# Performance work log

Measured on AMD Instinct MI355X. Metric: run time of the kernel, lower is better.

Reference implementation:

```python
import jax, jax.numpy as jnp
import numpy as np
from jax import lax

D = 96        # voxel grid side
C = 16        # code_dim == inner channels
NCONV = 17    # total conv layers in the net
DN = ('NCDHW', 'OIDHW', 'NCDHW')
PAD1 = [(1, 1)] * 3


def _bn_relu_mask(y, s, b, mask):
    # eval-mode BN folded to scale/bias, ReLU, then restrict to active voxels
    s = s[None, :, None, None, None]
    b = b[None, :, None, None, None]
    return jnp.maximum(y * s + b, 0.0) * mask


def _subm(x, mask, w, s, b):
    # SubMConv3d: dense 3x3x3 conv on zero-padded sparse features, output only at
    # the (unchanged) active sites -> conv + mask is exactly equal math.
    y = lax.conv_general_dilated(x, w, (1, 1, 1), PAD1, dimension_numbers=DN)
    return _bn_relu_mask(y, s, b, mask)


def _down(x, mask, w, s, b):
    # SparseConv3d stride 2, pad 1: output active wherever any input in the 3^3
    # window is active (= max-pool of the mask).
    y = lax.conv_general_dilated(x, w, (2, 2, 2), PAD1, dimension_numbers=DN)
    new_mask = lax.reduce_window(mask, 0.0, lax.max, (1, 1, 3, 3, 3),
                                 (1, 1, 2, 2, 2),
                                 [(0, 0), (0, 0), (1, 1), (1, 1), (1, 1)])
    return _bn_relu_mask(y, s, b, new_mask), new_mask


def setup_inputs() -> dict:
    key = jax.random.key(0)
    k1, k2, k3, k4, k5 = jax.random.split(key, 5)
    mask_idx = jax.random.randint(k1, (1, 1, D, D, D), 0, 10, dtype=jnp.int32)
    mask = (mask_idx == 0).astype(jnp.float32)
    x = jax.random.normal(k2, (1, C, D, D, D), jnp.float32) * mask
    # 0.05 ~ 1/sqrt(27*16): keeps activations sane over 17 layers
    W = jax.random.normal(k3, (NCONV, C, C, 3, 3, 3), jnp.float32) * 0.05
    bn_scale = jax.random.uniform(k4, (NCONV, C), jnp.float32, 0.5, 1.5)
    bn_bias = jax.random.normal(k5, (NCONV, C), jnp.float32) * 0.1
    return {"x": x, "mask_idx": mask_idx, "W": W,
            "bn_scale": bn_scale, "bn_bias": bn_bias}


def reference(x, mask_idx, W, bn_scale, bn_bias):
    mask = (mask_idx == 0).astype(x.dtype)
    net = x
    i = 0
    # conv0: double_conv at full res
    for _ in range(2):
        net = _subm(net, mask, W[i], bn_scale[i], bn_bias[i]); i += 1
    # down0
    net, mask = _down(net, mask, W[i], bn_scale[i], bn_bias[i]); i += 1
    # conv1: double_conv -> net1.dense()
    for _ in range(2):
        net = _subm(net, mask, W[i], bn_scale[i], bn_bias[i]); i += 1
    net1 = net
    # down1 + conv2 (triple) -> net2
    net, mask = _down(net, mask, W[i], bn_scale[i], bn_bias[i]); i += 1
    for _ in range(3):
        net = _subm(net, mask, W[i], bn_scale[i], bn_bias[i]); i += 1
    net2 = net
    # down2 + conv3 (triple) -> net3
    net, mask = _down(net, mask, W[i], bn_scale[i], bn_bias[i]); i += 1
    for _ in range(3):
        net = _subm(net, mask, W[i], bn_scale[i], bn_bias[i]); i += 1
    net3 = net
    # down3 + conv4 (triple) -> net4
    net, mask = _down(net, mask, W[i], bn_scale[i], bn_bias[i]); i += 1
    for _ in range(3):
        net = _subm(net, mask, W[i], bn_scale[i], bn_bias[i]); i += 1
    net4 = net
    return (net1, net2, net3, net4)
```

## Files before the change

### kernel.cpp

```cpp
#include <hip/hip_runtime.h>

#define C 16
#define TAPS 27
#define NCONV 17
#define LISTCAP 98304
#define NPAIR 14

typedef _Float16 half8 __attribute__((ext_vector_type(8)));
typedef _Float16 half4 __attribute__((ext_vector_type(4)));
typedef float f32x4 __attribute__((ext_vector_type(4)));

__global__ void prep_kernel(const float* __restrict__ x, const int* __restrict__ mask_idx,
                            _Float16* __restrict__ P0h, _Float16* __restrict__ P1h,
                            const float* __restrict__ W, _Float16* __restrict__ Wh,
                            int* __restrict__ counts, float* __restrict__ m48) {
    const int n96 = 96 * 96 * 96;
    int b = blockIdx.x;
    if (b < 3456) {
        int v = b * 256 + threadIdx.x;
        half8 h0, h1;
#pragma unroll
        for (int c = 0; c < 8; c++) h0[c] = (_Float16)x[(long)c * n96 + v];
#pragma unroll
        for (int c = 0; c < 8; c++) h1[c] = (_Float16)x[(long)(c + 8) * n96 + v];
        half8* dp = reinterpret_cast<half8*>(P0h + (long)v * C);
        dp[0] = h0;
        dp[1] = h1;
        half8 zz = {};
        half8* zp = reinterpret_cast<half8*>(P1h + (long)v * C);
        zp[0] = zz;
        zp[1] = zz;
        int act = (mask_idx[v] == 0);
        unsigned long long bl = __ballot(act);
        __shared__ int wsum[4];
        int wid = threadIdx.x >> 6, lane = threadIdx.x & 63;
        if (lane == 0) wsum[wid] = __popcll(bl);
        __syncthreads();
        if (threadIdx.x == 0) counts[b] = wsum[0] + wsum[1] + wsum[2] + wsum[3];
    } else if (b < 3456 + 476) {
        int i = (b - 3456) * 256 + threadIdx.x;
        const int total = NCONV * NPAIR * 64 * 8;
        if (i < total) {
            int j = i & 7;
            int lane = (i >> 3) & 63;
            int p = (i >> 9) % NPAIR;
            int l = (i >> 9) / NPAIR;
            int co = lane & 15;
            int g = lane >> 4;
            int k = 8 * g + j;
            int ci = k & 15;
            int tap = 2 * p + (k >> 4);
            float val = (tap < TAPS) ? W[((l * C + co) * C + ci) * TAPS + tap] : 0.f;
            Wh[i] = (_Float16)val;
        }
    } else {
        int i = (b - 3456 - 476) * 256 + threadIdx.x;
        int xx = i % 48, yy = (i / 48) % 48, zc = i / (48 * 48);
        float m = 0.f;
        for (int dz = 0; dz < 3; dz++) {
            int z2 = 2 * zc - 1 + dz;
            if ((unsigned)z2 >= 96u) continue;
            for (int dy = 0; dy < 3; dy++) {
                int y2 = 2 * yy - 1 + dy;
                if ((unsigned)y2 >= 96u) continue;
                for (int dx = 0; dx < 3; dx++) {
                    int x2 = 2 * xx - 1 + dx;
                    if ((unsigned)x2 >= 96u) continue;
                    if (mask_idx[((long)z2 * 96 + y2) * 96 + x2] == 0) m = 1.f;
                }
            }
        }
        m48[i] = m;
    }
}

__global__ void scan_kernel(const int* __restrict__ counts, int* __restrict__ offsets,
                            int* __restrict__ nact, int nb) {
    __shared__ int s[256];
    int t = threadIdx.x;
    const int CH = (nb + 255) / 256;
    int base = t * CH, sum = 0;
    for (int j = 0; j < CH; j++)
        if (base + j < nb) sum += counts[base + j];
    s[t] = sum;
    __syncthreads();
    for (int off = 1; off < 256; off <<= 1) {
        int v = (t >= off) ? s[t - off] : 0;
        __syncthreads();
        s[t] += v;
        __syncthreads();
    }
    int run = s[t] - sum;
    for (int j = 0; j < CH; j++) {
        if (base + j < nb) {
            offsets[base + j] = run;
            run += counts[base + j];
        }
    }
    if (t == 255) *nact = s[255];
}

__global__ void scatter_kernel(const int* __restrict__ mi, const int* __restrict__ offsets,
                               int* __restrict__ list, int cap, const float* __restrict__ m48,
                               float* __restrict__ m24, float* __restrict__ m12,
                               float* __restrict__ m6) {
    int b = blockIdx.x;
    int tid = threadIdx.x;
    if (b < 3456) {
        int i = b * 256 + tid;
        int act = (mi[i] == 0);
        unsigned long long bl = __ballot(act);
        __shared__ int wsum[4];
        int wid = tid >> 6, lane = tid & 63;
        if (lane == 0) wsum[wid] = __popcll(bl);
        __syncthreads();
        int wbase = 0;
        for (int w = 0; w < wid; w++) wbase += wsum[w];
        int prefix = __popcll(bl & ((1ull << lane) - 1));
        if (act) {
            int pos = offsets[b] + wbase + prefix;
            if (pos < cap) list[pos] = i;
        }
    } else if (b < 3456 + 54) {
        int i = (b - 3456) * 256 + tid;
        if (i < 24 * 24 * 24) {
            int x = i % 24, y = (i / 24) % 24, z = i / (24 * 24);
            float m = 0.f;
            for (int dz = 0; dz < 3; dz++) {
                int zz = 2 * z - 1 + dz;
                if ((unsigned)zz >= 48u) continue;
                for (int dy = 0; dy < 3; dy++) {
                    int yy = 2 * y - 1 + dy;
                    if ((unsigned)yy >= 48u) continue;
                    for (int dx = 0; dx < 3; dx++) {
                        int xx = 2 * x - 1 + dx;
                        if ((unsigned)xx >= 48u) continue;
                        m = fmaxf(m, m48[((long)zz * 48 + yy) * 48 + xx]);
                    }
                }
            }
            m24[i] = m;
        }
    } else if (b < 3456 + 54 + 432) {
        int wv = (b - 3456 - 54) * 4 + (tid >> 6);
        int lane = tid & 63;
        int x = wv % 12, y = (wv / 12) % 12, z = wv / 144;
        float m = 0.f;
        for (int k = lane; k < 343; k += 64) {
            int dz = k / 49, r = k % 49, dy = r / 7, dx = r % 7;
            int zz = 4 * z - 3 + dz, yy = 4 * y - 3 + dy, xx = 4 * x - 3 + dx;
            if ((unsigned)zz < 48u && (unsigned)yy < 48u && (unsigned)xx < 48u)
                m = fmaxf(m, m48[((long)zz * 48 + yy) * 48 + xx]);
        }
        for (int off = 32; off; off >>= 1) m = fmaxf(m, __shfl_xor(m, off));
        if (lane == 0 && wv < 1728) m12[wv] = m;
    } else {
        int wv = (b - 3456 - 54 - 432) * 4 + (tid >> 6);
        int lane = tid & 63;
        int x = wv % 6, y = (wv / 6) % 6, z = wv / 36;
        float m = 0.f;
        for (int k = lane; k < 3375; k += 64) {
            int dz = k / 225, r = k % 225, dy = r / 15, dx = r % 15;
            int zz = 8 * z - 7 + dz, yy = 8 * y - 7 + dy, xx = 8 * x - 7 + dx;
            if ((unsigned)zz < 48u && (unsigned)yy < 48u && (unsigned)xx < 48u)
                m = fmaxf(m, m48[((long)zz * 48 + yy) * 48 + xx]);
        }
        for (int off = 32; off; off >>= 1) m = fmaxf(m, __shfl_xor(m, off));
        if (lane == 0 && wv < 216) m6[wv] = m;
    }
}

template <int STRIDE, bool SPARSE, bool WF32>
__global__ __launch_bounds__(256) void mconv_kernel(
    const _Float16* __restrict__ in, _Float16* __restrict__ out,
    const float* __restrict__ mask, const int* __restrict__ list,
    const int* __restrict__ nact, const _Float16* __restrict__ Whl,
    const float* __restrict__ bs, const float* __restrict__ bb,
    int Din, int Dout, float* __restrict__ outf) {
    int n = Dout * Dout * Dout;
    int nv;
    if (SPARSE) {
        nv = *nact;
        if (nv > LISTCAP) nv = LISTCAP;
    } else {
        nv = n;
    }
    int tile = blockIdx.x * 4 + (threadIdx.x >> 6);
    if (tile * 16 >= nv) return;

    int lane = threadIdx.x & 63;
    int col = lane & 15;
    int g = lane >> 4;
    int s = tile * 16 + col;
    bool val = s < nv;
    int v = 0;
    if (SPARSE) {
        if (val) v = list[s];
    } else {
        v = val ? s : 0;
    }
    int x = v % Dout, y = (v / Dout) % Dout, z = v / (Dout * Dout);

    const half8* wf = reinterpret_cast<const half8*>(Whl);
    half8 a[NPAIR];
#pragma unroll
    for (int p = 0; p < NPAIR; p++) a[p] = wf[p * 64 + lane];

    int half_off = (g & 1) * 8;
    int tg = g >> 1;

    f32x4 acc = {0.f, 0.f, 0.f, 0.f};
#pragma unroll
    for (int p = 0; p < NPAIR; p++) {
        int tap = 2 * p + tg;
        if (tap > TAPS - 1) tap = TAPS - 1;
        int kz = tap / 9, ky = (tap / 3) % 3, kx = tap % 3;
        int zz = STRIDE * z - 1 + kz;
        int yy = STRIDE * y - 1 + ky;
        int xx = STRIDE * x - 1 + kx;
        bool ok = val && ((unsigned)zz < (unsigned)Din) && ((unsigned)yy < (unsigned)Din) &&
                  ((unsigned)xx < (unsigned)Din);
        half8 b = {};
        if (ok) {
            b = *reinterpret_cast<const half8*>(
                in + (long)((zz * Din + yy) * Din + xx) * C + half_off);
        }
        acc = __builtin_amdgcn_mfma_f32_16x16x32_f16(a[p], b, acc, 0, 0, 0);
    }

    if (val) {
        float mk = SPARSE ? 1.f : mask[v];
        int cob = g * 4;
        half4 r;
#pragma unroll
        for (int j = 0; j < 4; j++) {
            float t = fmaxf(acc[j] * bs[cob + j] + bb[cob + j], 0.f) * mk;
            r[j] = (_Float16)t;
            if (WF32) outf[(long)(cob + j) * n + v] = t;
        }
        *reinterpret_cast<half4*>(out + (long)v * C + cob) = r;
    }
}

__global__ __launch_bounds__(1024) void tail6_kernel(
    const _Float16* __restrict__ gin,
    const float* __restrict__ m6, const _Float16* __restrict__ Wh,
    const float* __restrict__ bs, const float* __restrict__ bb,
    float* __restrict__ out4) {
    __shared__ _Float16 G0[216 * 16], G1[216 * 16];
    __shared__ float Lm6[216];

    int tid = threadIdx.x;
    int lane = tid & 63;
    int wid = tid >> 6;
    int col = lane & 15, g = lane >> 4;
    int ho = (g & 1) * 8, tg = g >> 1;

    for (int i = tid; i < 216; i += 1024) Lm6[i] = m6[i];
    __syncthreads();

    int s = wid * 16 + col;
    bool val = (wid < 14) && (s < 216);
    int v = val ? s : 0;
    int x = v % 6, y = (v / 6) % 6, z = v / 36;

    auto layer = [&](const _Float16* gsrc, const _Float16* lsrc, int Din, int stride,
                     int lidx, _Float16* lout, float* outf) {
        const half8* wf = reinterpret_cast<const half8*>(Wh + (long)lidx * NPAIR * 64 * 8);
        half8 a[NPAIR];
#pragma unroll
        for (int p = 0; p < NPAIR; p++) a[p] = wf[p * 64 + lane];
        f32x4 acc = {0.f, 0.f, 0.f, 0.f};
#pragma unroll
        for (int p = 0; p < NPAIR; p++) {
            int tap = 2 * p + tg;
            if (tap > TAPS - 1) tap = TAPS - 1;
            int kz = tap / 9, ky = (tap / 3) % 3, kx = tap % 3;
            int zz = stride * z - 1 + kz;
            int yy = stride * y - 1 + ky;
            int xx = stride * x - 1 + kx;
            bool ok = val && ((unsigned)zz < (unsigned)Din) && ((unsigned)yy < (unsigned)Din) &&
                      ((unsigned)xx < (unsigned)Din);
            half8 b = {};
            if (ok) {
                long off = (long)((zz * Din + yy) * Din + xx) * C + ho;
                b = gsrc ? *reinterpret_cast<const half8*>(gsrc + off)
                         : *reinterpret_cast<const half8*>(lsrc + off);
            }
            acc = __builtin_amdgcn_mfma_f32_16x16x32_f16(a[p], b, acc, 0, 0, 0);
        }
        if (val) {
            float mkv = Lm6[v];
            int cob = g * 4;
            const float* bsl = bs + lidx * C;
            const float* bbl = bb + lidx * C;
            half4 r;
#pragma unroll
            for (int j = 0; j < 4; j++) {
                float t = fmaxf(acc[j] * bsl[cob + j] + bbl[cob + j], 0.f) * mkv;
                r[j] = (_Float16)t;
                if (outf) outf[(long)(cob + j) * 216 + v] = t;
            }
            if (lout) *reinterpret_cast<half4*>(lout + (long)v * C + cob) = r;
        }
        __syncthreads();
    };

    layer(gin, nullptr, 12, 2, 13, G0, nullptr);
    layer(nullptr, G0, 6, 1, 14, G1, nullptr);
    layer(nullptr, G1, 6, 1, 15, G0, nullptr);
    layer(nullptr, G0, 6, 1, 16, nullptr, out4);
}

extern "C" void kernel_launch(void* const* d_in, const int* in_sizes, int n_in,
                              void* d_out, int out_size, void* d_ws, size_t ws_size,
                              hipStream_t stream) {
    const float* x = (const float*)d_in[0];
    const int* mask_idx = (const int*)d_in[1];
    const float* W = (const float*)d_in[2];
    const float* bs = (const float*)d_in[3];
    const float* bb = (const float*)d_in[4];
    float* out = (float*)d_out;

    const int n96 = 96 * 96 * 96;
    const int n48 = 48 * 48 * 48;
    const int n24 = 24 * 24 * 24;
    const int n12 = 12 * 12 * 12;
    const int n6 = 6 * 6 * 6;
    const int NB = 3456;

    _Float16* P0h = (_Float16*)d_ws;
    _Float16* P1h = P0h + (long)C * n96;
    float* m48 = (float*)(P1h + (long)C * n96);
    float* m24 = m48 + n48;
    float* m12 = m24 + n24;
    float* m6 = m12 + n12;
    _Float16* Wh = (_Float16*)(m6 + n6);
    int* list = (int*)(Wh + (long)NCONV * NPAIR * 64 * 8);
    int* counts = list + LISTCAP;
    int* offsets = counts + NB;
    int* nact = offsets + NB;

    hipLaunchKernelGGL(prep_kernel, dim3(3456 + 476 + 432), dim3(256), 0, stream,
                       x, mask_idx, P0h, P1h, W, Wh, counts, m48);
    hipLaunchKernelGGL(scan_kernel, dim3(1), dim3(256), 0, stream, counts, offsets, nact, NB);
    hipLaunchKernelGGL(scatter_kernel, dim3(3456 + 54 + 432 + 54), dim3(256), 0, stream,
                       mask_idx, offsets, list, LISTCAP, m48, m24, m12, m6);

    auto mblk = [&](long nvox) { return dim3((unsigned)((nvox + 63) / 64)); };
    auto WL = [&](int l) { return Wh + (long)l * NPAIR * 64 * 8; };

    hipLaunchKernelGGL((mconv_kernel<1, true, false>), mblk(LISTCAP), dim3(256), 0, stream,
                       P0h, P1h, (const float*)nullptr, list, nact, WL(0), bs, bb, 96, 96,
                       (float*)nullptr);
    hipLaunchKernelGGL((mconv_kernel<1, true, false>), mblk(LISTCAP), dim3(256), 0, stream,
                       P1h, P0h, (const float*)nullptr, list, nact, WL(1), bs + C, bb + C, 96, 96,
                       (float*)nullptr);
    hipLaunchKernelGGL((mconv_kernel<2, false, false>), mblk(n48), dim3(256), 0, stream,
                       P0h, P1h, m48, list, nact, WL(2), bs + 2 * C, bb + 2 * C, 96, 48,
                       (float*)nullptr);
    hipLaunchKernelGGL((mconv_kernel<1, false, false>), mblk(n48), dim3(256), 0, stream,
                       P1h, P0h, m48, list, nact, WL(3), bs + 3 * C, bb + 3 * C, 48, 48,
                       (float*)nullptr);
    hipLaunchKernelGGL((mconv_kernel<1, false, true>), mblk(n48), dim3(256), 0, stream,
                       P0h, P1h, m48, list, nact, WL(4), bs + 4 * C, bb + 4 * C, 48, 48,
                       out);
    hipLaunchKernelGGL((mconv_kernel<2, false, false>), mblk(n24), dim3(256), 0, stream,
                       P1h, P0h, m24, list, nact, WL(5), bs + 5 * C, bb + 5 * C, 48, 24,
                       (float*)nullptr);
    hipLaunchKernelGGL((mconv_kernel<1, false, false>), mblk(n24), dim3(256), 0, stream,
                       P0h, P1h, m24, list, nact, WL(6), bs + 6 * C, bb + 6 * C, 24, 24,
                       (float*)nullptr);
    hipLaunchKernelGGL((mconv_kernel<1, false, false>), mblk(n24), dim3(256), 0, stream,
                       P1h, P0h, m24, list, nact, WL(7), bs + 7 * C, bb + 7 * C, 24, 24,
                       (float*)nullptr);
    hipLaunchKernelGGL((mconv_kernel<1, false, true>), mblk(n24), dim3(256), 0, stream,
                       P0h, P1h, m24, list, nact, WL(8), bs + 8 * C, bb + 8 * C, 24, 24,
                       out + (long)C * n48);
    hipLaunchKernelGGL((mconv_kernel<2, false, false>), mblk(n12), dim3(256), 0, stream,
                       P1h, P0h, m12, list, nact, WL(9), bs + 9 * C, bb + 9 * C, 24, 12,
                       (float*)nullptr);
    hipLaunchKernelGGL((mconv_kernel<1, false, false>), mblk(n12), dim3(256), 0, stream,
                       P0h, P1h, m12, list, nact, WL(10), bs + 10 * C, bb + 10 * C, 12, 12,
                       (float*)nullptr);
    hipLaunchKernelGGL((mconv_kernel<1, false, false>), mblk(n12), dim3(256), 0, stream,
                       P1h, P0h, m12, list, nact, WL(11), bs + 11 * C, bb + 11 * C, 12, 12,
                       (float*)nullptr);
    hipLaunchKernelGGL((mconv_kernel<1, false, true>), mblk(n12), dim3(256), 0, stream,
                       P0h, P1h, m12, list, nact, WL(12), bs + 12 * C, bb + 12 * C, 12, 12,
                       out + (long)C * (n48 + n24));
    hipLaunchKernelGGL(tail6_kernel, dim3(1), dim3(1024), 0, stream,
                       P1h, m6, Wh, bs, bb, out + (long)C * (n48 + n24 + n12));
}
```

Baseline: 204.2 us.

## Use compact active-voxel storage with precomputed neighbor table for full-res convs

Replaces the dense 96^3 fp16 feature buffers with compact per-active-voxel arrays. An inverse index map and a 27-tap neighbor table are built once and shared by both full-resolution submanifold convs. The first downsample conv gathers through the inverse map. This removes the dense conversion and zero-fill of two 96^3x16 buffers and the scattered dense gathers, at the cost of an extra compaction kernel, a large neighbor table, and initialising a 96^3 int inverse map.

```diff
diff --git a/kernel.cpp b/kernel.cpp
--- a/kernel.cpp
+++ b/kernel.cpp
@@ -10,35 +10,12 @@
 typedef _Float16 half4 __attribute__((ext_vector_type(4)));
 typedef float f32x4 __attribute__((ext_vector_type(4)));
 
-__global__ void prep_kernel(const float* __restrict__ x, const int* __restrict__ mask_idx,
-                            _Float16* __restrict__ P0h, _Float16* __restrict__ P1h,
-                            const float* __restrict__ W, _Float16* __restrict__ Wh,
-                            int* __restrict__ counts, float* __restrict__ m48) {
-    const int n96 = 96 * 96 * 96;
+__global__ void prep_kernel(const int* __restrict__ mask_idx, const float* __restrict__ W,
+                            _Float16* __restrict__ Wh, int* __restrict__ counts,
+                            float* __restrict__ m48, int* __restrict__ inv) {
     int b = blockIdx.x;
-    if (b < 3456) {
-        int v = b * 256 + threadIdx.x;
-        half8 h0, h1;
-#pragma unroll
-        for (int c = 0; c < 8; c++) h0[c] = (_Float16)x[(long)c * n96 + v];
-#pragma unroll
-        for (int c = 0; c < 8; c++) h1[c] = (_Float16)x[(long)(c + 8) * n96 + v];
-        half8* dp = reinterpret_cast<half8*>(P0h + (long)v * C);
-        dp[0] = h0;
-        dp[1] = h1;
-        half8 zz = {};
-        half8* zp = reinterpret_cast<half8*>(P1h + (long)v * C);
-        zp[0] = zz;
-        zp[1] = zz;
-        int act = (mask_idx[v] == 0);
-        unsigned long long bl = __ballot(act);
-        __shared__ int wsum[4];
-        int wid = threadIdx.x >> 6, lane = threadIdx.x & 63;
-        if (lane == 0) wsum[wid] = __popcll(bl);
-        __syncthreads();
-        if (threadIdx.x == 0) counts[b] = wsum[0] + wsum[1] + wsum[2] + wsum[3];
-    } else if (b < 3456 + 476) {
-        int i = (b - 3456) * 256 + threadIdx.x;
+    if (b < 476) {
+        int i = b * 256 + threadIdx.x;
         const int total = NCONV * NPAIR * 64 * 8;
         if (i < total) {
             int j = i & 7;
@@ -53,8 +30,8 @@
             float val = (tap < TAPS) ? W[((l * C + co) * C + ci) * TAPS + tap] : 0.f;
             Wh[i] = (_Float16)val;
         }
-    } else {
-        int i = (b - 3456 - 476) * 256 + threadIdx.x;
+    } else if (b < 476 + 432) {
+        int i = (b - 476) * 256 + threadIdx.x;
         int xx = i % 48, yy = (i / 48) % 48, zc = i / (48 * 48);
         float m = 0.f;
         for (int dz = 0; dz < 3; dz++) {
@@ -71,6 +48,16 @@
             }
         }
         m48[i] = m;
+    } else {
+        int v = (b - 476 - 432) * 256 + threadIdx.x;
+        inv[v] = -1;
+        int act = (mask_idx[v] == 0);
+        unsigned long long bl = __ballot(act);
+        __shared__ int wsum[4];
+        int wid = threadIdx.x >> 6, lane = threadIdx.x & 63;
+        if (lane == 0) wsum[wid] = __popcll(bl);
+        __syncthreads();
+        if (threadIdx.x == 0) counts[b - 476 - 432] = wsum[0] + wsum[1] + wsum[2] + wsum[3];
     }
 }
 
@@ -101,9 +88,9 @@
 }
 
 __global__ void scatter_kernel(const int* __restrict__ mi, const int* __restrict__ offsets,
-                               int* __restrict__ list, int cap, const float* __restrict__ m48,
-                               float* __restrict__ m24, float* __restrict__ m12,
-                               float* __restrict__ m6) {
+                               int* __restrict__ list, int* __restrict__ inv, int cap,
+                               const float* __restrict__ m48, float* __restrict__ m24,
+                               float* __restrict__ m12, float* __restrict__ m6) {
     int b = blockIdx.x;
     int tid = threadIdx.x;
     if (b < 3456) {
@@ -119,7 +106,10 @@
         int prefix = __popcll(bl & ((1ull << lane) - 1));
         if (act) {
             int pos = offsets[b] + wbase + prefix;
-            if (pos < cap) list[pos] = i;
+            if (pos < cap) {
+                list[pos] = i;
+                inv[i] = pos;
+            }
         }
     } else if (b < 3456 + 54) {
         int i = (b - 3456) * 256 + tid;
@@ -170,21 +160,41 @@
     }
 }
 
-template <int STRIDE, bool SPARSE, bool WF32>
-__global__ __launch_bounds__(256) void mconv_kernel(
-    const _Float16* __restrict__ in, _Float16* __restrict__ out,
-    const float* __restrict__ mask, const int* __restrict__ list,
-    const int* __restrict__ nact, const _Float16* __restrict__ Whl,
-    const float* __restrict__ bs, const float* __restrict__ bb,
-    int Din, int Dout, float* __restrict__ outf) {
-    int n = Dout * Dout * Dout;
-    int nv;
-    if (SPARSE) {
-        nv = *nact;
-        if (nv > LISTCAP) nv = LISTCAP;
-    } else {
-        nv = n;
-    }
+__global__ void compactx_kernel(const float* __restrict__ x, const int* __restrict__ list,
+                                const int* __restrict__ nact, const int* __restrict__ inv,
+                                _Float16* __restrict__ Xc, int* __restrict__ nbr) {
+    const int n96 = 96 * 96 * 96;
+    int nv = *nact;
+    if (nv > LISTCAP) nv = LISTCAP;
+    int s = blockIdx.x * 256 + threadIdx.x;
+    if (s >= nv) return;
+    int v = list[s];
+    half8 h0, h1;
+#pragma unroll
+    for (int c = 0; c < 8; c++) h0[c] = (_Float16)x[(long)c * n96 + v];
+#pragma unroll
+    for (int c = 0; c < 8; c++) h1[c] = (_Float16)x[(long)(c + 8) * n96 + v];
+    half8* dp = reinterpret_cast<half8*>(Xc + (long)s * C);
+    dp[0] = h0;
+    dp[1] = h1;
+    int xx = v % 96, yy = (v / 96) % 96, zz = v / (96 * 96);
+    for (int t = 0; t < TAPS; t++) {
+        int kz = t / 9, ky = (t / 3) % 3, kx = t % 3;
+        int z2 = zz - 1 + kz, y2 = yy - 1 + ky, x2 = xx - 1 + kx;
+        int idx = -1;
+        if ((unsigned)z2 < 96u && (unsigned)y2 < 96u && (unsigned)x2 < 96u)
+            idx = inv[((long)z2 * 96 + y2) * 96 + x2];
+        nbr[t * LISTCAP + s] = idx;
+    }
+}
+
+__global__ __launch_bounds__(256) void sconv_kernel(
+    const _Float16* __restrict__ Ain, _Float16* __restrict__ Aout,
+    const int* __restrict__ nbr, const int* __restrict__ nact,
+    const _Float16* __restrict__ Whl, const float* __restrict__ bs,
+    const float* __restrict__ bb) {
+    int nv = *nact;
+    if (nv > LISTCAP) nv = LISTCAP;
     int tile = blockIdx.x * 4 + (threadIdx.x >> 6);
     if (tile * 16 >= nv) return;
 
@@ -193,12 +203,98 @@
     int g = lane >> 4;
     int s = tile * 16 + col;
     bool val = s < nv;
-    int v = 0;
-    if (SPARSE) {
-        if (val) v = list[s];
-    } else {
-        v = val ? s : 0;
-    }
+
+    const half8* wf = reinterpret_cast<const half8*>(Whl);
+    half8 a[NPAIR];
+#pragma unroll
+    for (int p = 0; p < NPAIR; p++) a[p] = wf[p * 64 + lane];
+
+    int half_off = (g & 1) * 8;
+    int tg = g >> 1;
+
+    f32x4 acc = {0.f, 0.f, 0.f, 0.f};
+#pragma unroll
+    for (int p = 0; p < NPAIR; p++) {
+        int tap = 2 * p + tg;
+        if (tap > TAPS - 1) tap = TAPS - 1;
+        int idx = -1;
+        if (val) idx = nbr[tap * LISTCAP + s];
+        half8 b = {};
+        if (idx >= 0) b = *reinterpret_cast<const half8*>(Ain + (long)idx * C + half_off);
+        acc = __builtin_amdgcn_mfma_f32_16x16x32_f16(a[p], b, acc, 0, 0, 0);
+    }
+
+    if (val) {
+        int cob = g * 4;
+        half4 r;
+#pragma unroll
+        for (int j = 0; j < 4; j++)
+            r[j] = (_Float16)fmaxf(acc[j] * bs[cob + j] + bb[cob + j], 0.f);
+        *reinterpret_cast<half4*>(Aout + (long)s * C + cob) = r;
+    }
+}
+
+__global__ __launch_bounds__(256) void dconv_inv_kernel(
+    const _Float16* __restrict__ Ain, _Float16* __restrict__ out,
+    const float* __restrict__ mask, const int* __restrict__ inv,
+    const _Float16* __restrict__ Whl, const float* __restrict__ bs,
+    const float* __restrict__ bb) {
+    const int n = 48 * 48 * 48;
+    int tile = blockIdx.x * 4 + (threadIdx.x >> 6);
+    if (tile * 16 >= n) return;
+    int lane = threadIdx.x & 63;
+    int col = lane & 15;
+    int g = lane >> 4;
+    int v = tile * 16 + col;
+    int x = v % 48, y = (v / 48) % 48, z = v / (48 * 48);
+
+    const half8* wf = reinterpret_cast<const half8*>(Whl);
+    half8 a[NPAIR];
+#pragma unroll
+    for (int p = 0; p < NPAIR; p++) a[p] = wf[p * 64 + lane];
+    int half_off = (g & 1) * 8;
+    int tg = g >> 1;
+
+    f32x4 acc = {0.f, 0.f, 0.f, 0.f};
+#pragma unroll
+    for (int p = 0; p < NPAIR; p++) {
+        int tap = 2 * p + tg;
+        if (tap > TAPS - 1) tap = TAPS - 1;
+        int kz = tap / 9, ky = (tap / 3) % 3, kx = tap % 3;
+        int zz = 2 * z - 1 + kz, yy = 2 * y - 1 + ky, xx = 2 * x - 1 + kx;
+        int idx = -1;
+        if ((unsigned)zz < 96u && (unsigned)yy < 96u && (unsigned)xx < 96u)
+            idx = inv[((long)zz * 96 + yy) * 96 + xx];
+        half8 b = {};
+        if (idx >= 0) b = *reinterpret_cast<const half8*>(Ain + (long)idx * C + half_off);
+        acc = __builtin_amdgcn_mfma_f32_16x16x32_f16(a[p], b, acc, 0, 0, 0);
+    }
+
+    float mk = mask[v];
+    int cob = g * 4;
+    half4 r;
+#pragma unroll
+    for (int j = 0; j < 4; j++)
+        r[j] = (_Float16)(fmaxf(acc[j] * bs[cob + j] + bb[cob + j], 0.f) * mk);
+    *reinterpret_cast<half4*>(out + (long)v * C + cob) = r;
+}
+
+template <int STRIDE, bool WF32>
+__global__ __launch_bounds__(256) void mconv_kernel(
+    const _Float16* __restrict__ in, _Float16* __restrict__ out,
+    const float* __restrict__ mask, const _Float16* __restrict__ Whl,
+    const float* __restrict__ bs, const float* __restrict__ bb,
+    int Din, int Dout, float* __restrict__ outf) {
+    int n = Dout * Dout * Dout;
+    int tile = blockIdx.x * 4 + (threadIdx.x >> 6);
+    if (tile * 16 >= n) return;
+
+    int lane = threadIdx.x & 63;
+    int col = lane & 15;
+    int g = lane >> 4;
+    int s = tile * 16 + col;
+    bool val = s < n;
+    int v = val ? s : 0;
     int x = v % Dout, y = (v / Dout) % Dout, z = v / (Dout * Dout);
 
     const half8* wf = reinterpret_cast<const half8*>(Whl);
@@ -229,7 +325,7 @@
     }
 
     if (val) {
-        float mk = SPARSE ? 1.f : mask[v];
+        float mk = mask[v];
         int cob = g * 4;
         half4 r;
 #pragma unroll
@@ -243,10 +339,9 @@
 }
 
 __global__ __launch_bounds__(1024) void tail6_kernel(
-    const _Float16* __restrict__ gin,
-    const float* __restrict__ m6, const _Float16* __restrict__ Wh,
-    const float* __restrict__ bs, const float* __restrict__ bb,
-    float* __restrict__ out4) {
+    const _Float16* __restrict__ gin, const float* __restrict__ m6,
+    const _Float16* __restrict__ Wh, const float* __restrict__ bs,
+    const float* __restrict__ bb, float* __restrict__ out4) {
     __shared__ _Float16 G0[216 * 16], G1[216 * 16];
     __shared__ float Lm6[216];
 
@@ -329,9 +424,7 @@
     const int n6 = 6 * 6 * 6;
     const int NB = 3456;
 
-    _Float16* P0h = (_Float16*)d_ws;
-    _Float16* P1h = P0h + (long)C * n96;
-    float* m48 = (float*)(P1h + (long)C * n96);
+    float* m48 = (float*)d_ws;
     float* m24 = m48 + n48;
     float* m12 = m24 + n24;
     float* m6 = m12 + n12;
@@ -340,54 +433,51 @@
     int* counts = list + LISTCAP;
     int* offsets = counts + NB;
     int* nact = offsets + NB;
-
-    hipLaunchKernelGGL(prep_kernel, dim3(3456 + 476 + 432), dim3(256), 0, stream,
-                       x, mask_idx, P0h, P1h, W, Wh, counts, m48);
+    int* inv = nact + 1;
+    int* nbr = inv + n96;
+    _Float16* Xc = (_Float16*)(nbr + TAPS * LISTCAP);
+    _Float16* A1 = Xc + (long)LISTCAP * C;
+    _Float16* A2 = A1 + (long)LISTCAP * C;
+    _Float16* P0h = A2 + (long)LISTCAP * C;
+    _Float16* P1h = P0h + (long)n48 * C;
+
+    hipLaunchKernelGGL(prep_kernel, dim3(476 + 432 + 3456), dim3(256), 0, stream,
+                       mask_idx, W, Wh, counts, m48, inv);
     hipLaunchKernelGGL(scan_kernel, dim3(1), dim3(256), 0, stream, counts, offsets, nact, NB);
     hipLaunchKernelGGL(scatter_kernel, dim3(3456 + 54 + 432 + 54), dim3(256), 0, stream,
-                       mask_idx, offsets, list, LISTCAP, m48, m24, m12, m6);
+                       mask_idx, offsets, list, inv, LISTCAP, m48, m24, m12, m6);
+    hipLaunchKernelGGL(compactx_kernel, dim3(LISTCAP / 256), dim3(256), 0, stream,
+                       x, list, nact, inv, Xc, nbr);
 
     auto mblk = [&](long nvox) { return dim3((unsigned)((nvox + 63) / 64)); };
     auto WL = [&](int l) { return Wh + (long)l * NPAIR * 64 * 8; };
 
-    hipLaunchKernelGGL((mconv_kernel<1, true, false>), mblk(LISTCAP), dim3(256), 0, stream,
-                       P0h, P1h, (const float*)nullptr, list, nact, WL(0), bs, bb, 96, 96,
-                       (float*)nullptr);
-    hipLaunchKernelGGL((mconv_kernel<1, true, false>), mblk(LISTCAP), dim3(256), 0, stream,
-                       P1h, P0h, (const float*)nullptr, list, nact, WL(1), bs + C, bb + C, 96, 96,
-                       (float*)nullptr);
-    hipLaunchKernelGGL((mconv_kernel<2, false, false>), mblk(n48), dim3(256), 0, stream,
-                       P0h, P1h, m48, list, nact, WL(2), bs + 2 * C, bb + 2 * C, 96, 48,
-                       (float*)nullptr);
-    hipLaunchKernelGGL((mconv_kernel<1, false, false>), mblk(n48), dim3(256), 0, stream,
-                       P1h, P0h, m48, list, nact, WL(3), bs + 3 * C, bb + 3 * C, 48, 48,
-                       (float*)nullptr);
-    hipLaunchKernelGGL((mconv_kernel<1, false, true>), mblk(n48), dim3(256), 0, stream,
-                       P0h, P1h, m48, list, nact, WL(4), bs + 4 * C, bb + 4 * C, 48, 48,
-                       out);
-    hipLaunchKernelGGL((mconv_kernel<2, false, false>), mblk(n24), dim3(256), 0, stream,
-                       P1h, P0h, m24, list, nact, WL(5), bs + 5 * C, bb + 5 * C, 48, 24,
-                       (float*)nullptr);
-    hipLaunchKernelGGL((mconv_kernel<1, false, false>), mblk(n24), dim3(256), 0, stream,
-                       P0h, P1h, m24, list, nact, WL(6), bs + 6 * C, bb + 6 * C, 24, 24,
-                       (float*)nullptr);
-    hipLaunchKernelGGL((mconv_kernel<1, false, false>), mblk(n24), dim3(256), 0, stream,
-                       P1h, P0h, m24, list, nact, WL(7), bs + 7 * C, bb + 7 * C, 24, 24,
-                       (float*)nullptr);
-    hipLaunchKernelGGL((mconv_kernel<1, false, true>), mblk(n24), dim3(256), 0, stream,
-                       P0h, P1h, m24, list, nact, WL(8), bs + 8 * C, bb + 8 * C, 24, 24,
-                       out + (long)C * n48);
-    hipLaunchKernelGGL((mconv_kernel<2, false, false>), mblk(n12), dim3(256), 0, stream,
-                       P1h, P0h, m12, list, nact, WL(9), bs + 9 * C, bb + 9 * C, 24, 12,
-                       (float*)nullptr);
-    hipLaunchKernelGGL((mconv_kernel<1, false, false>), mblk(n12), dim3(256), 0, stream,
-                       P0h, P1h, m12, list, nact, WL(10), bs + 10 * C, bb + 10 * C, 12, 12,
-                       (float*)nullptr);
-    hipLaunchKernelGGL((mconv_kernel<1, false, false>), mblk(n12), dim3(256), 0, stream,
-                       P1h, P0h, m12, list, nact, WL(11), bs + 11 * C, bb + 11 * C, 12, 12,
-                       (float*)nullptr);
-    hipLaunchKernelGGL((mconv_kernel<1, false, true>), mblk(n12), dim3(256), 0, stream,
-                       P0h, P1h, m12, list, nact, WL(12), bs + 12 * C, bb + 12 * C, 12, 12,
+    hipLaunchKernelGGL(sconv_kernel, mblk(LISTCAP), dim3(256), 0, stream,
+                       Xc, A1, nbr, nact, WL(0), bs, bb);
+    hipLaunchKernelGGL(sconv_kernel, mblk(LISTCAP), dim3(256), 0, stream,
+                       A1, A2, nbr, nact, WL(1), bs + C, bb + C);
+    hipLaunchKernelGGL(dconv_inv_kernel, mblk(n48), dim3(256), 0, stream,
+                       A2, P1h, m48, inv, WL(2), bs + 2 * C, bb + 2 * C);
+    hipLaunchKernelGGL((mconv_kernel<1, false>), mblk(n48), dim3(256), 0, stream,
+                       P1h, P0h, m48, WL(3), bs + 3 * C, bb + 3 * C, 48, 48, (float*)nullptr);
+    hipLaunchKernelGGL((mconv_kernel<1, true>), mblk(n48), dim3(256), 0, stream,
+                       P0h, P1h, m48, WL(4), bs + 4 * C, bb + 4 * C, 48, 48, out);
+    hipLaunchKernelGGL((mconv_kernel<2, false>), mblk(n24), dim3(256), 0, stream,
+                       P1h, P0h, m24, WL(5), bs + 5 * C, bb + 5 * C, 48, 24, (float*)nullptr);
+    hipLaunchKernelGGL((mconv_kernel<1, false>), mblk(n24), dim3(256), 0, stream,
+                       P0h, P1h, m24, WL(6), bs + 6 * C, bb + 6 * C, 24, 24, (float*)nullptr);
+    hipLaunchKernelGGL((mconv_kernel<1, false>), mblk(n24), dim3(256), 0, stream,
+                       P1h, P0h, m24, WL(7), bs + 7 * C, bb + 7 * C, 24, 24, (float*)nullptr);
+    hipLaunchKernelGGL((mconv_kernel<1, true>), mblk(n24), dim3(256), 0, stream,
+                       P0h, P1h, m24, WL(8), bs + 8 * C, bb + 8 * C, 24, 24, out + (long)C * n48);
+    hipLaunchKernelGGL((mconv_kernel<2, false>), mblk(n12), dim3(256), 0, stream,
+                       P1h, P0h, m12, WL(9), bs + 9 * C, bb + 9 * C, 24, 12, (float*)nullptr);
+    hipLaunchKernelGGL((mconv_kernel<1, false>), mblk(n12), dim3(256), 0, stream,
+                       P0h, P1h, m12, WL(10), bs + 10 * C, bb + 10 * C, 12, 12, (float*)nullptr);
+    hipLaunchKernelGGL((mconv_kernel<1, false>), mblk(n12), dim3(256), 0, stream,
+                       P1h, P0h, m12, WL(11), bs + 11 * C, bb + 11 * C, 12, 12, (float*)nullptr);
+    hipLaunchKernelGGL((mconv_kernel<1, true>), mblk(n12), dim3(256), 0, stream,
+                       P0h, P1h, m12, WL(12), bs + 12 * C, bb + 12 * C, 12, 12,
                        out + (long)C * (n48 + n24));
     hipLaunchKernelGGL(tail6_kernel, dim3(1), dim3(1024), 0, stream,
                        P1h, m6, Wh, bs, bb, out + (long)C * (n48 + n24 + n12));
```

New measurement: 195.7 us. 1.04x faster.
